# Kernel optimization log

Measured on AMD Instinct MI355X. Metric: run time of the kernel, lower is better.

The kernel has to match this reference:

```python
import jax, jax.numpy as jnp
import numpy as np

H = 256
N = 200000
B = 2048
M = 6


def _lstm_cell(x, h, c, Wih, Whh, bih, bhh):
    # PyTorch LSTM gate order: i, f, g, o
    gates = x @ Wih.T + h @ Whh.T + bih + bhh  # [B, 4H]
    i, f, g, o = jnp.split(gates, 4, axis=1)
    i = jax.nn.sigmoid(i)
    f = jax.nn.sigmoid(f)
    g = jnp.tanh(g)
    o = jax.nn.sigmoid(o)
    c_new = f * c + i * g
    h_new = o * jnp.tanh(c_new)
    return h_new, c_new


def setup_inputs() -> dict:
    key = jax.random.key(0)
    ks = jax.random.split(key, 11)
    s = 1.0 / np.sqrt(H)  # pytorch LSTM init scale
    nodes = jax.random.normal(ks[0], (N, H), jnp.float32)
    graph_id = jnp.sort(jax.random.randint(ks[1], (N,), 0, B, dtype=jnp.int64))
    return {
        "nodes": nodes,
        "graph_id": graph_id,
        "num_graphs": B,
        "Wih0": jax.random.normal(ks[2], (4 * H, 2 * H), jnp.float32) * s,
        "Whh0": jax.random.normal(ks[3], (4 * H, H), jnp.float32) * s,
        "bih0": jax.random.normal(ks[4], (4 * H,), jnp.float32) * s,
        "bhh0": jax.random.normal(ks[5], (4 * H,), jnp.float32) * s,
        "Wih1": jax.random.normal(ks[6], (4 * H, H), jnp.float32) * s,
        "Whh1": jax.random.normal(ks[7], (4 * H, H), jnp.float32) * s,
        "bih1": jax.random.normal(ks[8], (4 * H,), jnp.float32) * s,
        "bhh1": jax.random.normal(ks[9], (4 * H,), jnp.float32) * s,
    }


def reference(nodes, graph_id, num_graphs, Wih0, Whh0, bih0, bhh0, Wih1, Whh1, bih1, bhh1):
    n_hidden = nodes.shape[1]
    dt = nodes.dtype
    h0 = jnp.zeros((num_graphs, n_hidden), dt)
    c0 = jnp.zeros((num_graphs, n_hidden), dt)
    h1 = jnp.zeros((num_graphs, n_hidden), dt)
    c1 = jnp.zeros((num_graphs, n_hidden), dt)
    q = jnp.zeros((num_graphs, n_hidden), dt)
    q_star = None
    for i in range(M):
        # attention logits per node: e_v = <nodes_v, q_{g(v)}>
        e = jnp.sum(nodes * q[graph_id], axis=1)  # [N]
        # segment softmax over each graph
        emax = jax.ops.segment_max(e, graph_id, num_segments=num_graphs)
        ex = jnp.exp(e - emax[graph_id])
        denom = jax.ops.segment_sum(ex, graph_id, num_segments=num_graphs)
        a = ex / denom[graph_id]  # [N]
        # attention-weighted readout per graph
        r = jax.ops.segment_sum(a[:, None] * nodes, graph_id, num_segments=num_graphs)  # [B, H]
        q_star = jnp.concatenate([q, r], axis=1)  # [B, 2H]
        if i < M - 1:
            h0, c0 = _lstm_cell(q_star, h0, c0, Wih0, Whh0, bih0, bhh0)
            h1, c1 = _lstm_cell(h0, h1, c1, Wih1, Whh1, bih1, bhh1)
            q = h1
    return q_star
```

## Files before the change

### kernel.cpp

```cpp
#include <hip/hip_runtime.h>
#include <hip/hip_bf16.h>
#include <cstdint>

#define HDIM 256

typedef __attribute__((ext_vector_type(8))) short bf16x8;
typedef __attribute__((ext_vector_type(4))) float f32x4;

__device__ __forceinline__ float bf2f(unsigned short u) {
    union { unsigned u; float f; } v; v.u = ((unsigned)u) << 16; return v.f;
}
__device__ __forceinline__ unsigned short f2bf(float f) {
    union { float f; unsigned u; } v; v.f = f;
    unsigned u = v.u;
    return (unsigned short)((u + 0x7fffu + ((u >> 16) & 1u)) >> 16);
}
__device__ __forceinline__ void gload_lds16(const void* g, void* l) {
    __builtin_amdgcn_global_load_lds((const __attribute__((address_space(1))) void*)g,
                                     (__attribute__((address_space(3))) void*)l, 16, 0, 0);
}
__device__ __forceinline__ float fsigm(float x) {
    return 1.f / (1.f + __expf(-x));
}
__device__ __forceinline__ float ftanh(float x) {
    float ax = fabsf(x);
    float z = __expf(2.f * ax);
    float th = 1.f - 2.f / (z + 1.f);
    return copysignf(th, x);
}

__global__ void k_prep(const float* __restrict__ Wih0, const float* __restrict__ Whh0,
                       const float* __restrict__ bih0, const float* __restrict__ bhh0,
                       const float* __restrict__ Wih1, const float* __restrict__ Whh1,
                       const float* __restrict__ bih1, const float* __restrict__ bhh1,
                       unsigned short* __restrict__ W0, unsigned short* __restrict__ W1,
                       float* __restrict__ b0, float* __restrict__ b1,
                       const int* __restrict__ gid, int* __restrict__ offs, int N, int B) {
    int idx = blockIdx.x * 256 + threadIdx.x;
    const int n0 = 1024 * 768, n1 = 1024 * 512;
    if (idx < n0) {
        int r = idx / 768, k = idx - r * 768;
        int orow = ((r >> 4) & 3) * 256 + ((r >> 6) << 4) + (r & 15);
        float v = (k < 512) ? Wih0[orow * 512 + k] : Whh0[orow * 256 + (k - 512)];
        W0[idx] = f2bf(v);
    } else if (idx < n0 + n1) {
        int j = idx - n0;
        int r = j >> 9, k = j & 511;
        int orow = ((r >> 4) & 3) * 256 + ((r >> 6) << 4) + (r & 15);
        float v = (k < 256) ? Wih1[orow * 256 + k] : Whh1[orow * 256 + (k - 256)];
        W1[j] = f2bf(v);
    } else if (idx < n0 + n1 + 1024) {
        int r = idx - (n0 + n1);
        int orow = ((r >> 4) & 3) * 256 + ((r >> 6) << 4) + (r & 15);
        b0[r] = bih0[orow] + bhh0[orow];
        b1[r] = bih1[orow] + bhh1[orow];
    } else if (idx <= n0 + n1 + 1024 + B) {
        int g = idx - (n0 + n1 + 1024);
        int lo = 0, hi = N;
        while (lo < hi) { int mid = (lo + hi) >> 1; if (gid[mid] < g) lo = mid + 1; else hi = mid; }
        offs[g] = lo;
    }
}

template<bool BF>
__global__ void __launch_bounds__(256) k_mean_cast(const float* __restrict__ nodes,
                                                   const int* __restrict__ offs,
                                                   unsigned short* __restrict__ nbf,
                                                   unsigned short* __restrict__ xr, int N) {
    __shared__ float red[4 * HDIM];
    int g = blockIdx.x, t = threadIdx.x;
    int lane = t & 63, wid = t >> 6;
    int start = offs[g], end = offs[g + 1];
    int Nm1 = N - 1;
    size_t col = (size_t)lane * 4;
    float4 acc = {0.f, 0.f, 0.f, 0.f};
    for (int vi0 = start + wid * 4; vi0 < end; vi0 += 16) {
        float4 v[4];
#pragma unroll
        for (int r = 0; r < 4; ++r)
            v[r] = *(const float4*)(nodes + (size_t)min(vi0 + r, Nm1) * HDIM + col);
#pragma unroll
        for (int r = 0; r < 4; ++r) {
            if (vi0 + r < end) {
                acc.x += v[r].x; acc.y += v[r].y; acc.z += v[r].z; acc.w += v[r].w;
                if (BF) {
                    ushort4 o; o.x = f2bf(v[r].x); o.y = f2bf(v[r].y);
                    o.z = f2bf(v[r].z); o.w = f2bf(v[r].w);
                    *(ushort4*)(nbf + (size_t)(vi0 + r) * HDIM + col) = o;
                }
            }
        }
    }
    *(float4*)(red + wid * HDIM + lane * 4) = acc;
    __syncthreads();
    int n = end - start;
    float r = red[t] + red[HDIM + t] + red[2 * HDIM + t] + red[3 * HDIM + t];
    r = (n > 0) ? r / (float)n : 0.f;
    xr[(size_t)g * 768 + HDIM + t] = f2bf(r);
}

template<bool LAST>
__global__ void __launch_bounds__(256) k_attn(const unsigned short* __restrict__ nb,
                                              const int* __restrict__ offs,
                                              const float* __restrict__ q,
                                              float* __restrict__ out,
                                              unsigned short* __restrict__ xr, int N) {
    __shared__ float qs[HDIM];
    __shared__ float redr[8 * HDIM];
    __shared__ float redm[8], redd[8];
    int g = blockIdx.x, t = threadIdx.x;
    int lane = t & 63, wid = t >> 6;
    int half = lane >> 5, hl = lane & 31;
    int start = offs[g], end = offs[g + 1];
    int Nm1 = N - 1;
    float qv = q[(size_t)g * HDIM + t];
    qs[t] = qv;
    __syncthreads();
    float qv8[8];
#pragma unroll
    for (int j = 0; j < 8; ++j) qv8[j] = qs[hl * 8 + j];
    float m = -INFINITY, d = 0.f, racc[8];
#pragma unroll
    for (int j = 0; j < 8; ++j) racc[j] = 0.f;
    size_t col = (size_t)hl * 8;
    int vi0 = start + wid * 4;
    bf16x8 cura = *(const bf16x8*)(nb + (size_t)min(vi0 + half, Nm1) * HDIM + col);
    bf16x8 curb = *(const bf16x8*)(nb + (size_t)min(vi0 + 2 + half, Nm1) * HDIM + col);
    for (; vi0 < end; vi0 += 16) {
        int nvi = vi0 + 16;
        bf16x8 nxta = *(const bf16x8*)(nb + (size_t)min(nvi + half, Nm1) * HDIM + col);
        bf16x8 nxtb = *(const bf16x8*)(nb + (size_t)min(nvi + 2 + half, Nm1) * HDIM + col);
        int a = vi0 + half, b = a + 2;
        if (a < end) {
            float xa[8], xb[8];
#pragma unroll
            for (int j = 0; j < 8; ++j) {
                xa[j] = bf2f((unsigned short)cura[j]);
                xb[j] = bf2f((unsigned short)curb[j]);
            }
            float ea = 0.f, eb = 0.f;
#pragma unroll
            for (int j = 0; j < 8; ++j) {
                ea = fmaf(qv8[j], xa[j], ea);
                eb = fmaf(qv8[j], xb[j], eb);
            }
#pragma unroll
            for (int o = 16; o >= 1; o >>= 1) {
                ea += __shfl_xor(ea, o, 64);
                eb += __shfl_xor(eb, o, 64);
            }
            if (b >= end) eb = -INFINITY;
            float nm = fmaxf(fmaxf(m, ea), eb);
            float sc = __expf(m - nm);
            float wa = __expf(ea - nm);
            float wb = __expf(eb - nm);
            m = nm;
            d = fmaf(d, sc, wa + wb);
#pragma unroll
            for (int j = 0; j < 8; ++j)
                racc[j] = fmaf(racc[j], sc, fmaf(wa, xa[j], wb * xb[j]));
        }
        cura = nxta; curb = nxtb;
    }
    int g2 = wid * 2 + half;
    *(float4*)(redr + g2 * HDIM + hl * 8)     = (float4){racc[0], racc[1], racc[2], racc[3]};
    *(float4*)(redr + g2 * HDIM + hl * 8 + 4) = (float4){racc[4], racc[5], racc[6], racc[7]};
    if (hl == 0) { redm[g2] = m; redd[g2] = d; }
    __syncthreads();
    float M = -INFINITY;
#pragma unroll
    for (int i = 0; i < 8; ++i) M = fmaxf(M, redm[i]);
    float D = 0.f, R = 0.f;
#pragma unroll
    for (int i = 0; i < 8; ++i) {
        float s = (redm[i] == -INFINITY) ? 0.f : __expf(redm[i] - M);
        D += redd[i] * s;
        R += redr[i * HDIM + t] * s;
    }
    float r = (D > 0.f) ? R / D : 0.f;
    if (LAST) {
        size_t ob = (size_t)g * (2 * HDIM);
        out[ob + t] = qv;
        out[ob + HDIM + t] = r;
    } else {
        xr[(size_t)g * 768 + HDIM + t] = f2bf(r);
    }
}

template<bool LAST>
__global__ void __launch_bounds__(256) k_attn_f32(const float* __restrict__ nf,
                                                  const int* __restrict__ offs,
                                                  const float* __restrict__ q,
                                                  float* __restrict__ out,
                                                  unsigned short* __restrict__ xr) {
    __shared__ float qs[HDIM];
    __shared__ float redr[4 * HDIM];
    __shared__ float redm[4], redd[4];
    int g = blockIdx.x, t = threadIdx.x;
    int lane = t & 63, wid = t >> 6;
    int start = offs[g], end = offs[g + 1];
    float qv = q[(size_t)g * HDIM + t];
    qs[t] = qv;
    __syncthreads();
    float4 qq = *(const float4*)(qs + lane * 4);
    float m = -INFINITY, d = 0.f;
    float4 racc = {0.f, 0.f, 0.f, 0.f};
    for (int vi = start + wid; vi < end; vi += 4) {
        float4 x = *(const float4*)(nf + (size_t)vi * HDIM + lane * 4);
        float e = qq.x * x.x + qq.y * x.y + qq.z * x.z + qq.w * x.w;
#pragma unroll
        for (int o = 32; o >= 1; o >>= 1) e += __shfl_xor(e, o, 64);
        float nm = fmaxf(m, e);
        float sc = __expf(m - nm);
        float wv = __expf(e - nm);
        m = nm;
        d = d * sc + wv;
        racc.x = racc.x * sc + wv * x.x;
        racc.y = racc.y * sc + wv * x.y;
        racc.z = racc.z * sc + wv * x.z;
        racc.w = racc.w * sc + wv * x.w;
    }
    *(float4*)(redr + wid * HDIM + lane * 4) = racc;
    if (lane == 0) { redm[wid] = m; redd[wid] = d; }
    __syncthreads();
    float M = fmaxf(fmaxf(redm[0], redm[1]), fmaxf(redm[2], redm[3]));
    float D = 0.f, R = 0.f;
#pragma unroll
    for (int i = 0; i < 4; ++i) {
        float s = (redm[i] == -INFINITY) ? 0.f : __expf(redm[i] - M);
        D += redd[i] * s;
        R += redr[i * HDIM + t] * s;
    }
    float r = (D > 0.f) ? R / D : 0.f;
    if (LAST) {
        size_t ob = (size_t)g * (2 * HDIM);
        out[ob + t] = qv;
        out[ob + HDIM + t] = r;
    } else {
        xr[(size_t)g * 768 + HDIM + t] = f2bf(r);
    }
}

template<int K, int PHASE>
__global__ void __launch_bounds__(256) k_gemm_lstm(const unsigned short* __restrict__ A,
                                                   const unsigned short* __restrict__ W,
                                                   const float* __restrict__ bias_p,
                                                   float* __restrict__ c,
                                                   unsigned short* __restrict__ xa,
                                                   unsigned short* __restrict__ xb,
                                                   float* __restrict__ qout) {
    __shared__ unsigned short lA[64 * 32];
    __shared__ unsigned short lB[128 * 32];
    int t = threadIdx.x, lane = t & 63, wid = t >> 6;
    int wy = wid >> 1, wx = wid & 1;
    int brow = blockIdx.x * 64, bcol = blockIdx.y * 128;
    f32x4 acc[2][4];
#pragma unroll
    for (int i = 0; i < 2; ++i)
#pragma unroll
        for (int j = 0; j < 4; ++j) acc[i][j] = (f32x4){0.f, 0.f, 0.f, 0.f};
    int sr = t >> 2, sc = (t & 3) * 8;
    for (int k0 = 0; k0 < K; k0 += 32) {
        gload_lds16(A + (size_t)(brow + sr) * K + k0 + sc, lA + t * 8);
        gload_lds16(W + (size_t)(bcol + sr) * K + k0 + sc, lB + t * 8);
        gload_lds16(W + (size_t)(bcol + 64 + sr) * K + k0 + sc, lB + 2048 + t * 8);
        asm volatile("s_waitcnt vmcnt(0)" ::: "memory");
        __syncthreads();
        bf16x8 af[2], bfr[4];
#pragma unroll
        for (int mm = 0; mm < 2; ++mm)
            af[mm] = *(const bf16x8*)(lA + (wy * 32 + mm * 16 + (lane & 15)) * 32 + (lane >> 4) * 8);
#pragma unroll
        for (int nn = 0; nn < 4; ++nn)
            bfr[nn] = *(const bf16x8*)(lB + (wx * 64 + nn * 16 + (lane & 15)) * 32 + (lane >> 4) * 8);
#pragma unroll
        for (int mm = 0; mm < 2; ++mm)
#pragma unroll
            for (int nn = 0; nn < 4; ++nn)
                acc[mm][nn] = __builtin_amdgcn_mfma_f32_16x16x32_bf16(af[mm], bfr[nn], acc[mm][nn], 0, 0, 0);
        __syncthreads();
    }
    int f = lane & 15;
    int cg = bcol + wx * 64 + f;
    float bi = bias_p[cg], bff = bias_p[cg + 16], bg = bias_p[cg + 32], bo = bias_p[cg + 48];
    int feat = (blockIdx.y * 2 + wx) * 16 + f;
#pragma unroll
    for (int mm = 0; mm < 2; ++mm)
#pragma unroll
        for (int j = 0; j < 4; ++j) {
            int row = brow + wy * 32 + mm * 16 + (lane >> 4) * 4 + j;
            float gi = fsigm(acc[mm][0][j] + bi);
            float gf = fsigm(acc[mm][1][j] + bff);
            float gg = ftanh(acc[mm][2][j] + bg);
            float go = fsigm(acc[mm][3][j] + bo);
            size_t idx = (size_t)row * HDIM + feat;
            float cn_ = gf * c[idx] + gi * gg;
            c[idx] = cn_;
            float h = go * ftanh(cn_);
            unsigned short hb = f2bf(h);
            if (PHASE == 0) {
                xa[(size_t)row * 768 + 512 + feat] = hb;
                xb[(size_t)row * 512 + feat] = hb;
            } else {
                qout[idx] = h;
                xa[(size_t)row * 768 + feat] = hb;
                xb[(size_t)row * 512 + 256 + feat] = hb;
            }
        }
}

extern "C" void kernel_launch(void* const* d_in, const int* in_sizes, int n_in,
                              void* d_out, int out_size, void* d_ws, size_t ws_size,
                              hipStream_t stream) {
    const float* nodes = (const float*)d_in[0];
    const int* gid = (const int*)d_in[1];
    const float* Wih0 = (const float*)d_in[3];
    const float* Whh0 = (const float*)d_in[4];
    const float* bih0 = (const float*)d_in[5];
    const float* bhh0 = (const float*)d_in[6];
    const float* Wih1 = (const float*)d_in[7];
    const float* Whh1 = (const float*)d_in[8];
    const float* bih1 = (const float*)d_in[9];
    const float* bhh1 = (const float*)d_in[10];
    int N = in_sizes[0] / HDIM;
    int B = out_size / (2 * HDIM);
    float* out = (float*)d_out;

    const size_t AL = 512;
    auto rnd = [&](size_t b) { return (b + AL - 1) & ~(AL - 1); };
    size_t offs_b  = rnd((size_t)(B + 1) * 4);
    size_t q_b     = rnd((size_t)B * HDIM * 4);
    size_t xb0_b   = rnd((size_t)B * 768 * 2);
    size_t xb1_b   = rnd((size_t)B * 512 * 2);
    size_t w0_b    = rnd((size_t)1024 * 768 * 2);
    size_t w1_b    = rnd((size_t)1024 * 512 * 2);
    size_t bias_b  = rnd((size_t)1024 * 4);
    size_t nb_b    = rnd((size_t)N * HDIM * 2);
    size_t base_need = offs_b + 3 * q_b + 2 * xb0_b + 2 * xb1_b + w0_b + w1_b + 2 * bias_b;
    bool useBF = (base_need + nb_b <= ws_size);

    char* w = (char*)d_ws;
    unsigned short* nodes_bf = nullptr;
    if (useBF) { nodes_bf = (unsigned short*)w; w += nb_b; }
    int* offs = (int*)w;               w += offs_b;
    float* q  = (float*)w;             w += q_b;
    float* c0 = (float*)w;             w += q_b;
    float* c1 = (float*)w;             w += q_b;
    unsigned short* xb0v[2]; unsigned short* xb1v[2];
    xb0v[0] = (unsigned short*)w;      w += xb0_b;
    xb0v[1] = (unsigned short*)w;      w += xb0_b;
    xb1v[0] = (unsigned short*)w;      w += xb1_b;
    xb1v[1] = (unsigned short*)w;      w += xb1_b;
    unsigned short* W0 = (unsigned short*)w;  w += w0_b;
    unsigned short* W1 = (unsigned short*)w;  w += w1_b;
    float* b0 = (float*)w;             w += bias_b;
    float* b1 = (float*)w;             w += bias_b;

    hipMemsetAsync(q,  0, (size_t)B * HDIM * 4, stream);
    hipMemsetAsync(c0, 0, (size_t)B * HDIM * 4, stream);
    hipMemsetAsync(c1, 0, (size_t)B * HDIM * 4, stream);
    hipMemsetAsync(xb0v[0], 0, (size_t)B * 768 * 2, stream);
    hipMemsetAsync(xb1v[0], 0, (size_t)B * 512 * 2, stream);

    {
        int total = 1024 * 768 + 1024 * 512 + 1024 + B + 1;
        k_prep<<<dim3((total + 255) / 256), dim3(256), 0, stream>>>(
            Wih0, Whh0, bih0, bhh0, Wih1, Whh1, bih1, bhh1, W0, W1, b0, b1,
            gid, offs, N, B);
    }
    if (useBF)
        k_mean_cast<true><<<dim3(B), dim3(256), 0, stream>>>(nodes, offs, nodes_bf, xb0v[0], N);
    else
        k_mean_cast<false><<<dim3(B), dim3(256), 0, stream>>>(nodes, offs, nullptr, xb0v[0], N);

    for (int s = 0; s < 5; ++s) {
        int vr = s & 1, vw = vr ^ 1;
        k_gemm_lstm<768, 0><<<dim3(B / 64, 8), dim3(256), 0, stream>>>(
            xb0v[vr], W0, b0, c0, xb0v[vw], xb1v[vr], nullptr);
        k_gemm_lstm<512, 1><<<dim3(B / 64, 8), dim3(256), 0, stream>>>(
            xb1v[vr], W1, b1, c1, xb0v[vw], xb1v[vw], q);
        if (s < 4) {
            if (useBF)
                k_attn<false><<<dim3(B), dim3(256), 0, stream>>>(nodes_bf, offs, q, nullptr, xb0v[vw], N);
            else
                k_attn_f32<false><<<dim3(B), dim3(256), 0, stream>>>(nodes, offs, q, nullptr, xb0v[vw]);
        } else {
            if (useBF)
                k_attn<true><<<dim3(B), dim3(256), 0, stream>>>(nodes_bf, offs, q, out, nullptr, N);
            else
                k_attn_f32<true><<<dim3(B), dim3(256), 0, stream>>>(nodes, offs, q, out, nullptr);
        }
    }
}
```

Before: 320.1 us.

## Triple-buffer GEMM K-loop with swizzled LDS and fold memsets into mean kernel

The LSTM GEMM kernel moves to a BK=64 tile with a three-stage LDS ring buffer. Loads for tile t+2 are issued before the MFMAs on tile t, and partial vmcnt waits replace the full drain, so global loads overlap compute. LDS chunks are XOR-swizzled to reduce bank conflicts. The five separate memsets for state buffers are removed, and the mean/cast kernel now zeroes c0, c1 and the unused activation slices itself, saving launches. This raises LDS use per block, which may lower occupancy, and the q buffer is no longer zeroed.

```diff
diff --git a/kernel.cpp b/kernel.cpp
--- a/kernel.cpp
+++ b/kernel.cpp
@@ -66,7 +66,10 @@
 __global__ void __launch_bounds__(256) k_mean_cast(const float* __restrict__ nodes,
                                                    const int* __restrict__ offs,
                                                    unsigned short* __restrict__ nbf,
-                                                   unsigned short* __restrict__ xr, int N) {
+                                                   unsigned short* __restrict__ xr,
+                                                   unsigned short* __restrict__ xb1z,
+                                                   float* __restrict__ c0,
+                                                   float* __restrict__ c1, int N) {
     __shared__ float red[4 * HDIM];
     int g = blockIdx.x, t = threadIdx.x;
     int lane = t & 63, wid = t >> 6;
@@ -96,7 +99,12 @@
     int n = end - start;
     float r = red[t] + red[HDIM + t] + red[2 * HDIM + t] + red[3 * HDIM + t];
     r = (n > 0) ? r / (float)n : 0.f;
+    xr[(size_t)g * 768 + t] = 0;
     xr[(size_t)g * 768 + HDIM + t] = f2bf(r);
+    xr[(size_t)g * 768 + 512 + t] = 0;
+    xb1z[(size_t)g * 512 + 256 + t] = 0;
+    c0[(size_t)g * HDIM + t] = 0.f;
+    c1[(size_t)g * HDIM + t] = 0.f;
 }
 
 template<bool LAST>
@@ -249,8 +257,10 @@
                                                    unsigned short* __restrict__ xa,
                                                    unsigned short* __restrict__ xb,
                                                    float* __restrict__ qout) {
-    __shared__ unsigned short lA[64 * 32];
-    __shared__ unsigned short lB[128 * 32];
+    constexpr int BK = 64;
+    constexpr int NT = K / BK;
+    __shared__ unsigned short lA[3 * 64 * BK];
+    __shared__ unsigned short lB[3 * 128 * BK];
     int t = threadIdx.x, lane = t & 63, wid = t >> 6;
     int wy = wid >> 1, wx = wid & 1;
     int brow = blockIdx.x * 64, bcol = blockIdx.y * 128;
@@ -259,26 +269,66 @@
     for (int i = 0; i < 2; ++i)
 #pragma unroll
         for (int j = 0; j < 4; ++j) acc[i][j] = (f32x4){0.f, 0.f, 0.f, 0.f};
-    int sr = t >> 2, sc = (t & 3) * 8;
-    for (int k0 = 0; k0 < K; k0 += 32) {
-        gload_lds16(A + (size_t)(brow + sr) * K + k0 + sc, lA + t * 8);
-        gload_lds16(W + (size_t)(bcol + sr) * K + k0 + sc, lB + t * 8);
-        gload_lds16(W + (size_t)(bcol + 64 + sr) * K + k0 + sc, lB + 2048 + t * 8);
-        asm volatile("s_waitcnt vmcnt(0)" ::: "memory");
-        __syncthreads();
-        bf16x8 af[2], bfr[4];
-#pragma unroll
-        for (int mm = 0; mm < 2; ++mm)
-            af[mm] = *(const bf16x8*)(lA + (wy * 32 + mm * 16 + (lane & 15)) * 32 + (lane >> 4) * 8);
-#pragma unroll
-        for (int nn = 0; nn < 4; ++nn)
-            bfr[nn] = *(const bf16x8*)(lB + (wx * 64 + nn * 16 + (lane & 15)) * 32 + (lane >> 4) * 8);
-#pragma unroll
-        for (int mm = 0; mm < 2; ++mm)
-#pragma unroll
-            for (int nn = 0; nn < 4; ++nn)
-                acc[mm][nn] = __builtin_amdgcn_mfma_f32_16x16x32_bf16(af[mm], bfr[nn], acc[mm][nn], 0, 0, 0);
-        __syncthreads();
+    const unsigned short* gA = A + (size_t)brow * K;
+    const unsigned short* gW = W + (size_t)bcol * K;
+    auto stage = [&](int tt, int b) {
+        int k0 = tt * BK;
+        unsigned short* dA = lA + b * (64 * BK);
+        unsigned short* dB = lB + b * (128 * BK);
+#pragma unroll
+        for (int r = 0; r < 2; ++r) {
+            int u = t + r * 256;
+            int row = u >> 3, sc8 = (u & 7) ^ (row & 7);
+            gload_lds16(gA + (size_t)row * K + k0 + sc8 * 8, dA + u * 8);
+        }
+#pragma unroll
+        for (int r = 0; r < 4; ++r) {
+            int u = t + r * 256;
+            int row = u >> 3, sc8 = (u & 7) ^ (row & 7);
+            gload_lds16(gW + (size_t)row * K + k0 + sc8 * 8, dB + u * 8);
+        }
+    };
+    stage(0, 0);
+    stage(1, 1);
+    asm volatile("s_waitcnt vmcnt(6)" ::: "memory");
+    __builtin_amdgcn_s_barrier();
+    int arow = wy * 32 + (lane & 15);
+    int brow2 = wx * 64 + (lane & 15);
+    int gc8 = lane >> 4;
+#pragma unroll
+    for (int tt = 0; tt < NT; ++tt) {
+        const unsigned short* bA = lA + (tt % 3) * (64 * BK);
+        const unsigned short* bB = lB + (tt % 3) * (128 * BK);
+        bf16x8 af[2][2], bfr[2][4];
+#pragma unroll
+        for (int kh = 0; kh < 2; ++kh) {
+#pragma unroll
+            for (int mm = 0; mm < 2; ++mm) {
+                int row = arow + mm * 16;
+                int ch = (gc8 + kh * 4) ^ (row & 7);
+                af[kh][mm] = *(const bf16x8*)(bA + row * BK + ch * 8);
+            }
+#pragma unroll
+            for (int nn = 0; nn < 4; ++nn) {
+                int row = brow2 + nn * 16;
+                int ch = (gc8 + kh * 4) ^ (row & 7);
+                bfr[kh][nn] = *(const bf16x8*)(bB + row * BK + ch * 8);
+            }
+        }
+        if (tt + 2 < NT) stage(tt + 2, (tt + 2) % 3);
+#pragma unroll
+        for (int kh = 0; kh < 2; ++kh)
+#pragma unroll
+            for (int mm = 0; mm < 2; ++mm)
+#pragma unroll
+                for (int nn = 0; nn < 4; ++nn)
+                    acc[mm][nn] = __builtin_amdgcn_mfma_f32_16x16x32_bf16(
+                        af[kh][mm], bfr[kh][nn], acc[mm][nn], 0, 0, 0);
+        if (tt + 1 < NT) {
+            if (tt + 2 < NT) asm volatile("s_waitcnt vmcnt(6)" ::: "memory");
+            else             asm volatile("s_waitcnt vmcnt(0)" ::: "memory");
+            __builtin_amdgcn_s_barrier();
+        }
     }
     int f = lane & 15;
     int cg = bcol + wx * 64 + f;
@@ -356,12 +406,6 @@
     float* b0 = (float*)w;             w += bias_b;
     float* b1 = (float*)w;             w += bias_b;
 
-    hipMemsetAsync(q,  0, (size_t)B * HDIM * 4, stream);
-    hipMemsetAsync(c0, 0, (size_t)B * HDIM * 4, stream);
-    hipMemsetAsync(c1, 0, (size_t)B * HDIM * 4, stream);
-    hipMemsetAsync(xb0v[0], 0, (size_t)B * 768 * 2, stream);
-    hipMemsetAsync(xb1v[0], 0, (size_t)B * 512 * 2, stream);
-
     {
         int total = 1024 * 768 + 1024 * 512 + 1024 + B + 1;
         k_prep<<<dim3((total + 255) / 256), dim3(256), 0, stream>>>(
@@ -369,9 +413,11 @@
             gid, offs, N, B);
     }
     if (useBF)
-        k_mean_cast<true><<<dim3(B), dim3(256), 0, stream>>>(nodes, offs, nodes_bf, xb0v[0], N);
+        k_mean_cast<true><<<dim3(B), dim3(256), 0, stream>>>(nodes, offs, nodes_bf,
+                                                             xb0v[0], xb1v[0], c0, c1, N);
     else
-        k_mean_cast<false><<<dim3(B), dim3(256), 0, stream>>>(nodes, offs, nullptr, xb0v[0], N);
+        k_mean_cast<false><<<dim3(B), dim3(256), 0, stream>>>(nodes, offs, nullptr,
+                                                              xb0v[0], xb1v[0], c0, c1, N);
 
     for (int s = 0; s < 5; ++s) {
         int vr = s & 1, vw = vr ^ 1;
```

New measurement: 268.5 us. 16.1% less time.
